# Performance work log

Measured on AMD Instinct MI355X. Metric: run time of the kernel, lower is better.

The kernel has to match this reference:

```python
import jax, jax.numpy as jnp
import numpy as np

N = 100000   # nodes
E = 1600000  # edges
D = 128      # d_model
H = 8        # heads
HD = D // H  # head dim
T = 8        # edge types


def setup_inputs() -> dict:
    key = jax.random.key(0)
    ks = jax.random.split(key, 16)
    s = 0.02
    inp = {
        "x": jax.random.normal(ks[0], (N, D), jnp.float32),
        "edge_index": jax.random.randint(ks[1], (2, E), 0, N, jnp.int32),
        "edge_type": jax.random.randint(ks[2], (E,), 0, T, jnp.int32),
        "Wq": jax.random.normal(ks[3], (D, D), jnp.float32) * s,
        "bq": jnp.zeros((D,), jnp.float32),
        "Wk": jax.random.normal(ks[4], (D, D), jnp.float32) * s,
        "bk": jnp.zeros((D,), jnp.float32),
        "Wv": jax.random.normal(ks[5], (D, D), jnp.float32) * s,
        "bv": jnp.zeros((D,), jnp.float32),
        "Wo": jax.random.normal(ks[6], (D, D), jnp.float32) * s,
        "bo": jnp.zeros((D,), jnp.float32),
        "edge_bias": jax.random.normal(ks[7], (T, H), jnp.float32) * s,
        "W1": jax.random.normal(ks[8], (D, D), jnp.float32) * s,
        "b1": jnp.zeros((D,), jnp.float32),
        "W2": jax.random.normal(ks[9], (D, D), jnp.float32) * s,
        "b2": jnp.zeros((D,), jnp.float32),
        "g1": jnp.ones((D,), jnp.float32),
        "be1": jnp.zeros((D,), jnp.float32),
        "g2": jnp.ones((D,), jnp.float32),
        "be2": jnp.zeros((D,), jnp.float32),
    }
    return inp


def _layernorm(x, g, b, eps=1e-5):
    m = jnp.mean(x, axis=-1, keepdims=True)
    v = jnp.mean((x - m) ** 2, axis=-1, keepdims=True)
    return (x - m) * jax.lax.rsqrt(v + eps) * g + b


def reference(x, edge_index, edge_type, Wq, bq, Wk, bk, Wv, bv, Wo, bo,
              edge_bias, W1, b1, W2, b2, g1, be1, g2, be2):
    n = x.shape[0]
    scale = HD ** -0.5
    Q = (x @ Wq + bq).reshape(n, H, HD)
    K = (x @ Wk + bk).reshape(n, H, HD)
    V = (x @ Wv + bv).reshape(n, H, HD)
    src, dst = edge_index[0], edge_index[1]
    # per-edge attention logits [E, H]
    attn = jnp.sum(Q[dst] * K[src], axis=-1) * scale + edge_bias[edge_type]
    # segment softmax grouped by destination node
    mx = jax.ops.segment_max(attn, dst, num_segments=n)  # [n, H]
    ex = jnp.exp(attn - mx[dst])
    sm = jax.ops.segment_sum(ex, dst, num_segments=n)
    a = ex / (sm[dst] + 1e-16)
    # weighted scatter-add of values
    out = jax.ops.segment_sum(a[..., None] * V[src], dst, num_segments=n)
    out = out.reshape(n, D) @ Wo + bo
    x = _layernorm(x + out, g1, be1)
    ffn = jax.nn.gelu(x @ W1 + b1, approximate=False) @ W2 + b2
    return _layernorm(x + ffn, g2, be2)
```

## Files before the change

### kernel.cpp

```cpp
#include <hip/hip_runtime.h>
#include <math.h>

#define D   128
#define NH  8
#define CAP 64
#define SCW 132

typedef __attribute__((ext_vector_type(8))) short  bfrag;
typedef __attribute__((ext_vector_type(4))) float  f32x4;
typedef __attribute__((ext_vector_type(8))) unsigned short u16x8;

__device__ __forceinline__ unsigned short f2bf(float f) {
  unsigned int u = __float_as_uint(f);
  unsigned int r = u + 0x7fffu + ((u >> 16) & 1u);
  return (unsigned short)(r >> 16);
}
__device__ __forceinline__ float bf2f(unsigned short b) {
  return __uint_as_float(((unsigned int)b) << 16);
}

__device__ __forceinline__ int swz(int r, int kb) {
  return r * 256 + (kb ^ ((r & 7) << 4));
}

__global__ void prew_kernel(const float* __restrict__ W0, const float* __restrict__ W1,
                            const float* __restrict__ W2, const float* __restrict__ W3,
                            const float* __restrict__ W4, const float* __restrict__ W5,
                            unsigned short* __restrict__ img)
{
  const float* Wm[6] = {W0, W1, W2, W3, W4, W5};
  const float* W = Wm[blockIdx.x];
  unsigned short* ih = img + (size_t)blockIdx.x * 32768;
  unsigned short* il = ih + 16384;
  for (int s = threadIdx.x; s < 16384; s += 256) {
    int j = s & 7, l = (s >> 3) & 63, kk = (s >> 9) & 3, cbg = s >> 11;
    int c = cbg * 16 + (l & 15);
    int k = kk * 32 + (l >> 4) * 8 + j;
    float v = W[k * D + c];
    unsigned short h = f2bf(v);
    ih[s] = h;
    il[s] = f2bf(v - bf2f(h));
  }
}

__device__ __forceinline__ void stage_x(const float* __restrict__ A, char* lds,
                                        int r0, int n, int t)
{
#pragma unroll
  for (int i = 0; i < 8; ++i) {
    int f = i * 256 + t;
    int r = f >> 5;
    int c = (f & 31) * 4;
    float4 v = make_float4(0.f, 0.f, 0.f, 0.f);
    int row = r0 + r;
    if (row < n) v = *(const float4*)&A[(size_t)row * D + c];
    unsigned short h0 = f2bf(v.x), h1 = f2bf(v.y), h2 = f2bf(v.z), h3 = f2bf(v.w);
    ushort4 hv; hv.x = h0; hv.y = h1; hv.z = h2; hv.w = h3;
    ushort4 lv;
    lv.x = f2bf(v.x - bf2f(h0)); lv.y = f2bf(v.y - bf2f(h1));
    lv.z = f2bf(v.z - bf2f(h2)); lv.w = f2bf(v.w - bf2f(h3));
    int o = swz(r, c * 2);
    *(ushort4*)(lds + o)         = hv;
    *(ushort4*)(lds + 16384 + o) = lv;
  }
}

__device__ __forceinline__ void gemm_tile(const unsigned short* __restrict__ imgh,
                                          const unsigned short* __restrict__ imgl,
                                          const char* lds, f32x4 (&acc)[4][2],
                                          int wave, int lane)
{
  bfrag bh[2][4], bl[2][4];
#pragma unroll
  for (int cb = 0; cb < 2; ++cb)
#pragma unroll
    for (int kk = 0; kk < 4; ++kk) {
      int f = ((wave * 2 + cb) * 4 + kk) * 64 + lane;
      bh[cb][kk] = *(const bfrag*)&imgh[f * 8];
      bl[cb][kk] = *(const bfrag*)&imgl[f * 8];
    }
#pragma unroll
  for (int rb = 0; rb < 4; ++rb)
#pragma unroll
    for (int kk = 0; kk < 4; ++kk) {
      int o = swz(rb * 16 + (lane & 15), kk * 64 + (lane >> 4) * 16);
      bfrag ah = *(const bfrag*)(lds + o);
      bfrag al = *(const bfrag*)(lds + 16384 + o);
#pragma unroll
      for (int cb = 0; cb < 2; ++cb) {
        acc[rb][cb] = __builtin_amdgcn_mfma_f32_16x16x32_bf16(ah, bh[cb][kk], acc[rb][cb], 0, 0, 0);
        acc[rb][cb] = __builtin_amdgcn_mfma_f32_16x16x32_bf16(al, bh[cb][kk], acc[rb][cb], 0, 0, 0);
        acc[rb][cb] = __builtin_amdgcn_mfma_f32_16x16x32_bf16(ah, bl[cb][kk], acc[rb][cb], 0, 0, 0);
      }
    }
}

__device__ __forceinline__ void zero_acc(f32x4 (&acc)[4][2]) {
#pragma unroll
  for (int rb = 0; rb < 4; ++rb)
#pragma unroll
    for (int cb = 0; cb < 2; ++cb) {
      f32x4 z = {0.f, 0.f, 0.f, 0.f};
      acc[rb][cb] = z;
    }
}

__device__ __forceinline__ void store_scF(const f32x4 (&acc)[4][2], float* scF,
                                          const float* __restrict__ bias,
                                          int wave, int lane)
{
  float b0 = bias[wave * 32 + (lane & 15)];
  float b1 = bias[wave * 32 + 16 + (lane & 15)];
#pragma unroll
  for (int rb = 0; rb < 4; ++rb)
#pragma unroll
    for (int cb = 0; cb < 2; ++cb) {
      float bb = cb ? b1 : b0;
      int col = wave * 32 + cb * 16 + (lane & 15);
#pragma unroll
      for (int r = 0; r < 4; ++r) {
        int row = rb * 16 + (lane >> 4) * 4 + r;
        scF[row * SCW + col] = acc[rb][cb][r] + bb;
      }
    }
}

__device__ __forceinline__ void write_bufA4(char* lds, int row, int tc,
                                            float v0, float v1, float v2, float v3)
{
  unsigned short h0 = f2bf(v0), h1 = f2bf(v1), h2 = f2bf(v2), h3 = f2bf(v3);
  ushort4 hv; hv.x = h0; hv.y = h1; hv.z = h2; hv.w = h3;
  ushort4 lv;
  lv.x = f2bf(v0 - bf2f(h0)); lv.y = f2bf(v1 - bf2f(h1));
  lv.z = f2bf(v2 - bf2f(h2)); lv.w = f2bf(v3 - bf2f(h3));
  int o = swz(row, tc * 8);
  *(ushort4*)(lds + o)         = hv;
  *(ushort4*)(lds + 16384 + o) = lv;
}

__global__ __launch_bounds__(256, 2) void qkv_kernel(
    const float* __restrict__ x, const unsigned short* __restrict__ img,
    const float* __restrict__ bq, const float* __restrict__ bk, const float* __restrict__ bv,
    unsigned short* __restrict__ Q, unsigned short* __restrict__ K,
    unsigned short* __restrict__ V, int n)
{
  __shared__ char lds[49152];
  const int t = threadIdx.x, wave = t >> 6, lane = t & 63;
  const int r0 = blockIdx.x * 64;
  stage_x(x, lds, r0, n, t);
  __syncthreads();

  const float* bs[3] = {bq, bk, bv};
  unsigned short* Os[3] = {Q, K, V};
  unsigned short* scH = (unsigned short*)(lds + 32768);

  for (int m = 0; m < 3; ++m) {
    f32x4 acc[4][2];
    zero_acc(acc);
    gemm_tile(img + (size_t)m * 32768, img + (size_t)m * 32768 + 16384, lds, acc, wave, lane);
    float b0 = bs[m][wave * 32 + (lane & 15)];
    float b1 = bs[m][wave * 32 + 16 + (lane & 15)];
    __syncthreads();
#pragma unroll
    for (int rb = 0; rb < 4; ++rb)
#pragma unroll
      for (int cb = 0; cb < 2; ++cb) {
        float bb = cb ? b1 : b0;
        int col = wave * 32 + cb * 16 + (lane & 15);
#pragma unroll
        for (int r = 0; r < 4; ++r) {
          int row = rb * 16 + (lane >> 4) * 4 + r;
          scH[row * D + col] = f2bf(acc[rb][cb][r] + bb);
        }
      }
    __syncthreads();
#pragma unroll
    for (int i = 0; i < 8; ++i) {
      int f = i * 256 + t;
      int row = f >> 5, c4 = (f & 31) * 4;
      if (r0 + row < n)
        *(ushort4*)&Os[m][(size_t)(r0 + row) * D + c4] = *(ushort4*)&scH[row * D + c4];
    }
  }
}

__global__ __launch_bounds__(256, 2) void ffn_kernel(
    const float* __restrict__ AO, const unsigned short* __restrict__ img,
    const float* __restrict__ x,
    const float* __restrict__ bo, const float* __restrict__ b1, const float* __restrict__ b2,
    const float* __restrict__ g1, const float* __restrict__ be1,
    const float* __restrict__ g2, const float* __restrict__ be2,
    float* __restrict__ out, int n)
{
  __shared__ char lds[32768 + 64 * SCW * 4];
  float* scF = (float*)(lds + 32768);
  const int t = threadIdx.x, wave = t >> 6, lane = t & 63;
  const int r0 = blockIdx.x * 64;
  const int tc = t & 31, tr = t >> 5;

  stage_x(AO, lds, r0, n, t);
  __syncthreads();

  f32x4 acc[4][2];

  zero_acc(acc);
  gemm_tile(img + 3 * 32768, img + 3 * 32768 + 16384, lds, acc, wave, lane);
  store_scF(acc, scF, bo, wave, lane);
  __syncthreads();

  float x1v[8][4];
  {
    float4 g4  = *(const float4*)&g1[tc * 4];
    float4 be4 = *(const float4*)&be1[tc * 4];
#pragma unroll
    for (int i = 0; i < 8; ++i) {
      int row = tr * 8 + i, grow = r0 + row;
      float4 y = *(float4*)&scF[row * SCW + tc * 4];
      float4 rv = make_float4(0.f, 0.f, 0.f, 0.f);
      if (grow < n) rv = *(const float4*)&x[(size_t)grow * D + tc * 4];
      float y0 = y.x + rv.x, y1 = y.y + rv.y, y2 = y.z + rv.z, y3 = y.w + rv.w;
      float sum = y0 + y1 + y2 + y3;
#pragma unroll
      for (int off = 16; off; off >>= 1) sum += __shfl_xor(sum, off);
      float mean = sum * (1.f / 128.f);
      float d0 = y0 - mean, d1 = y1 - mean, d2 = y2 - mean, d3 = y3 - mean;
      float sq = d0 * d0 + d1 * d1 + d2 * d2 + d3 * d3;
#pragma unroll
      for (int off = 16; off; off >>= 1) sq += __shfl_xor(sq, off);
      float inv = 1.0f / sqrtf(sq * (1.f / 128.f) + 1e-5f);
      float v0 = d0 * inv * g4.x + be4.x, v1 = d1 * inv * g4.y + be4.y;
      float v2 = d2 * inv * g4.z + be4.z, v3 = d3 * inv * g4.w + be4.w;
      x1v[i][0] = v0; x1v[i][1] = v1; x1v[i][2] = v2; x1v[i][3] = v3;
      write_bufA4(lds, row, tc, v0, v1, v2, v3);
    }
  }
  __syncthreads();

  zero_acc(acc);
  gemm_tile(img + 4 * 32768, img + 4 * 32768 + 16384, lds, acc, wave, lane);
  store_scF(acc, scF, b1, wave, lane);
  __syncthreads();
#pragma unroll
  for (int i = 0; i < 8; ++i) {
    int row = tr * 8 + i;
    float4 y = *(float4*)&scF[row * SCW + tc * 4];
    const float kc = 0.70710678118654752f;
    float v0 = 0.5f * y.x * (1.f + erff(y.x * kc));
    float v1 = 0.5f * y.y * (1.f + erff(y.y * kc));
    float v2 = 0.5f * y.z * (1.f + erff(y.z * kc));
    float v3 = 0.5f * y.w * (1.f + erff(y.w * kc));
    write_bufA4(lds, row, tc, v0, v1, v2, v3);
  }
  __syncthreads();

  zero_acc(acc);
  gemm_tile(img + 5 * 32768, img + 5 * 32768 + 16384, lds, acc, wave, lane);
  store_scF(acc, scF, b2, wave, lane);
  __syncthreads();
  {
    float4 g4  = *(const float4*)&g2[tc * 4];
    float4 be4 = *(const float4*)&be2[tc * 4];
#pragma unroll
    for (int i = 0; i < 8; ++i) {
      int row = tr * 8 + i, grow = r0 + row;
      float4 y = *(float4*)&scF[row * SCW + tc * 4];
      float y0 = y.x + x1v[i][0], y1 = y.y + x1v[i][1];
      float y2 = y.z + x1v[i][2], y3 = y.w + x1v[i][3];
      float sum = y0 + y1 + y2 + y3;
#pragma unroll
      for (int off = 16; off; off >>= 1) sum += __shfl_xor(sum, off);
      float mean = sum * (1.f / 128.f);
      float d0 = y0 - mean, d1 = y1 - mean, d2 = y2 - mean, d3 = y3 - mean;
      float sq = d0 * d0 + d1 * d1 + d2 * d2 + d3 * d3;
#pragma unroll
      for (int off = 16; off; off >>= 1) sq += __shfl_xor(sq, off);
      float inv = 1.0f / sqrtf(sq * (1.f / 128.f) + 1e-5f);
      if (grow < n) {
        float4 o;
        o.x = d0 * inv * g4.x + be4.x; o.y = d1 * inv * g4.y + be4.y;
        o.z = d2 * inv * g4.z + be4.z; o.w = d3 * inv * g4.w + be4.w;
        *(float4*)&out[(size_t)grow * D + tc * 4] = o;
      }
    }
  }
}

__global__ __launch_bounds__(256) void fill_kernel(
    const int* __restrict__ ei, const int* __restrict__ et,
    int* __restrict__ cnt, unsigned* __restrict__ bucket,
    int n, int e, int nper)
{
  const int xcd = blockIdx.x & 7;
  const int lo  = xcd * nper;
  const int nb  = gridDim.x >> 3;
  const int sl  = blockIdx.x >> 3;
  const int stride = nb * 256;
  for (int i = sl * 256 + threadIdx.x; i < e; i += stride) {
    int d = ei[e + i];
    if ((unsigned)(d - lo) < (unsigned)nper) {
      int s  = ei[i];
      int ty = et[i];
      int pos = atomicAdd(&cnt[d], 1);
      if (pos < CAP) bucket[(size_t)d * CAP + pos] = (unsigned)s | ((unsigned)ty << 24);
    }
  }
}

__global__ __launch_bounds__(256) void attn_kernel(
    const unsigned short* __restrict__ Q, const unsigned short* __restrict__ K,
    const unsigned short* __restrict__ V, const float* __restrict__ ebias,
    const int* __restrict__ cnt, const unsigned* __restrict__ bucket,
    float* __restrict__ out, int n)
{
  __shared__ float eb_s[64];
  if (threadIdx.x < 64) eb_s[threadIdx.x] = ebias[threadIdx.x];
  __syncthreads();

  const int wave = threadIdx.x >> 6, lane = threadIdx.x & 63;
  const int node = blockIdx.x * 4 + wave;
  if (node >= n) return;

  const int g  = lane >> 4;
  const int l  = lane & 15;
  const int d0 = l * 8;
  const int h  = l >> 1;

  int deg = cnt[node];
  if (deg > CAP) deg = CAP;

  unsigned packed = 0u;
  if (lane < deg) packed = bucket[(size_t)node * CAP + lane];

  u16x8 qv = *(const u16x8*)&Q[(size_t)node * D + d0];
  float q[8];
#pragma unroll
  for (int i = 0; i < 8; ++i) q[i] = bf2f(qv[i]) * 0.25f;

  float s = 0.f, a[8];
#pragma unroll
  for (int i = 0; i < 8; ++i) a[i] = 0.f;

  for (int j = 0; j < deg; j += 4) {
    int slot = j + g;
    unsigned cur = __shfl(packed, slot < 63 ? slot : 63);
    int src = (int)(cur & 0xFFFFFFu);
    int ty  = (int)(cur >> 24);
    u16x8 kv = *(const u16x8*)&K[(size_t)src * D + d0];
    u16x8 vv = *(const u16x8*)&V[(size_t)src * D + d0];
    float dot = 0.f;
#pragma unroll
    for (int i = 0; i < 8; ++i) dot += q[i] * bf2f(kv[i]);
    dot += __shfl_xor(dot, 1);
    float logit = dot + eb_s[ty * NH + h];
    float p = (slot < deg) ? __expf(logit) : 0.f;
    s += p;
#pragma unroll
    for (int i = 0; i < 8; ++i) a[i] += p * bf2f(vv[i]);
  }
  s += __shfl_xor(s, 16); s += __shfl_xor(s, 32);
#pragma unroll
  for (int i = 0; i < 8; ++i) { a[i] += __shfl_xor(a[i], 16); a[i] += __shfl_xor(a[i], 32); }

  if (g == 0) {
    float inv = 1.f / (s + 1e-16f);
    float4 o0 = make_float4(a[0] * inv, a[1] * inv, a[2] * inv, a[3] * inv);
    float4 o1 = make_float4(a[4] * inv, a[5] * inv, a[6] * inv, a[7] * inv);
    *(float4*)&out[(size_t)node * D + d0]     = o0;
    *(float4*)&out[(size_t)node * D + d0 + 4] = o1;
  }
}

extern "C" void kernel_launch(void* const* d_in, const int* in_sizes, int n_in,
                              void* d_out, int out_size, void* d_ws, size_t ws_size,
                              hipStream_t stream)
{
  const float* x   = (const float*)d_in[0];
  const int*   ei  = (const int*)  d_in[1];
  const int*   et  = (const int*)  d_in[2];
  const float* Wq  = (const float*)d_in[3];
  const float* bq  = (const float*)d_in[4];
  const float* Wk  = (const float*)d_in[5];
  const float* bk  = (const float*)d_in[6];
  const float* Wv  = (const float*)d_in[7];
  const float* bv  = (const float*)d_in[8];
  const float* Wo  = (const float*)d_in[9];
  const float* bo  = (const float*)d_in[10];
  const float* eb  = (const float*)d_in[11];
  const float* W1  = (const float*)d_in[12];
  const float* b1  = (const float*)d_in[13];
  const float* W2  = (const float*)d_in[14];
  const float* b2  = (const float*)d_in[15];
  const float* g1  = (const float*)d_in[16];
  const float* be1 = (const float*)d_in[17];
  const float* g2  = (const float*)d_in[18];
  const float* be2 = (const float*)d_in[19];

  const int n = in_sizes[0] / D;
  const int e = in_sizes[2];
  const size_t nd = (size_t)n * D;

  unsigned short* Qb = (unsigned short*)d_ws;
  unsigned short* Kb = Qb + nd;
  unsigned short* Vb = Kb + nd;
  float*    AO     = (float*)(Vb + nd);
  unsigned* bucket = (unsigned*)(AO + nd);
  int*      cnt    = (int*)(bucket + (size_t)n * CAP);
  unsigned short* img = (unsigned short*)(cnt + n);

  hipMemsetAsync(cnt, 0, (size_t)n * sizeof(int), stream);

  const int gb = (n + 63) / 64;
  const int nper = (n + 7) / 8;
  prew_kernel<<<6, 256, 0, stream>>>(Wq, Wk, Wv, Wo, W1, W2, img);
  fill_kernel<<<2048, 256, 0, stream>>>(ei, et, cnt, bucket, n, e, nper);
  qkv_kernel<<<gb, 256, 0, stream>>>(x, img, bq, bk, bv, Qb, Kb, Vb, n);
  attn_kernel<<<(n + 3) / 4, 256, 0, stream>>>(Qb, Kb, Vb, eb, cnt, bucket, AO, n);
  ffn_kernel<<<gb, 256, 0, stream>>>(AO, img, x, bo, b1, b2, g1, be1, g2, be2,
                                     (float*)d_out, n);
}
```

Before: 488.8 us.

## Store K in FP8 and merge edge bucketing into the QKV kernel launch

K is now written as FP8 (e4m3 via the cvt_pk_fp8 builtin) instead of bf16, which halves the bytes gathered per edge for the key in the attention kernel. The attention kernel unpacks the FP8 values with cvt_pk_f32_fp8. The edge-bucketing fill work moves into extra blocks of the QKV GEMM launch so the two run concurrently, and the separate launch goes away. FP8 keys lose precision in the attention logits, which may push the error past tolerance, and the fill blocks' loop stride is hardcoded to 65536 assuming 2048 blocks.

```diff
diff --git a/kernel.cpp b/kernel.cpp
--- a/kernel.cpp
+++ b/kernel.cpp
@@ -8,6 +8,7 @@
 
 typedef __attribute__((ext_vector_type(8))) short  bfrag;
 typedef __attribute__((ext_vector_type(4))) float  f32x4;
+typedef __attribute__((ext_vector_type(2))) float  f32x2;
 typedef __attribute__((ext_vector_type(8))) unsigned short u16x8;
 
 __device__ __forceinline__ unsigned short f2bf(float f) {
@@ -138,21 +139,40 @@
   *(ushort4*)(lds + 16384 + o) = lv;
 }
 
-__global__ __launch_bounds__(256, 2) void qkv_kernel(
+__global__ __launch_bounds__(256, 2) void qkvf_kernel(
     const float* __restrict__ x, const unsigned short* __restrict__ img,
     const float* __restrict__ bq, const float* __restrict__ bk, const float* __restrict__ bv,
-    unsigned short* __restrict__ Q, unsigned short* __restrict__ K,
-    unsigned short* __restrict__ V, int n)
+    unsigned short* __restrict__ Q, unsigned char* __restrict__ K8,
+    unsigned short* __restrict__ V, int n, int gb,
+    const int* __restrict__ ei, const int* __restrict__ et,
+    int* __restrict__ cnt, unsigned* __restrict__ bucket, int e, int nper)
 {
   __shared__ char lds[49152];
-  const int t = threadIdx.x, wave = t >> 6, lane = t & 63;
+  const int t = threadIdx.x;
+
+  if ((int)blockIdx.x >= gb) {
+    const int bid = blockIdx.x - gb;
+    const int xcd = bid & 7;
+    const int lo  = xcd * nper;
+    const int sl  = bid >> 3;
+    for (int i = sl * 256 + t; i < e; i += 65536) {
+      int d = ei[e + i];
+      if ((unsigned)(d - lo) < (unsigned)nper) {
+        int s  = ei[i];
+        int ty = et[i];
+        int pos = atomicAdd(&cnt[d], 1);
+        if (pos < CAP) bucket[(size_t)d * CAP + pos] = (unsigned)s | ((unsigned)ty << 24);
+      }
+    }
+    return;
+  }
+
+  const int wave = t >> 6, lane = t & 63;
   const int r0 = blockIdx.x * 64;
   stage_x(x, lds, r0, n, t);
   __syncthreads();
 
   const float* bs[3] = {bq, bk, bv};
-  unsigned short* Os[3] = {Q, K, V};
-  unsigned short* scH = (unsigned short*)(lds + 32768);
 
   for (int m = 0; m < 3; ++m) {
     f32x4 acc[4][2];
@@ -161,25 +181,53 @@
     float b0 = bs[m][wave * 32 + (lane & 15)];
     float b1 = bs[m][wave * 32 + 16 + (lane & 15)];
     __syncthreads();
-#pragma unroll
-    for (int rb = 0; rb < 4; ++rb)
-#pragma unroll
-      for (int cb = 0; cb < 2; ++cb) {
-        float bb = cb ? b1 : b0;
-        int col = wave * 32 + cb * 16 + (lane & 15);
-#pragma unroll
-        for (int r = 0; r < 4; ++r) {
-          int row = rb * 16 + (lane >> 4) * 4 + r;
-          scH[row * D + col] = f2bf(acc[rb][cb][r] + bb);
+    if (m == 1) {
+      unsigned char* scB = (unsigned char*)(lds + 32768);
+#pragma unroll
+      for (int rb = 0; rb < 4; ++rb)
+#pragma unroll
+        for (int cb = 0; cb < 2; ++cb) {
+          float bb = cb ? b1 : b0;
+          int col = wave * 32 + cb * 16 + (lane & 15);
+#pragma unroll
+          for (int r = 0; r < 4; ++r) {
+            int row = rb * 16 + (lane >> 4) * 4 + r;
+            float v = acc[rb][cb][r] + bb;
+            unsigned p = (unsigned)__builtin_amdgcn_cvt_pk_fp8_f32(v, v, 0, false);
+            scB[row * 128 + col] = (unsigned char)(p & 0xFF);
+          }
         }
-      }
-    __syncthreads();
-#pragma unroll
-    for (int i = 0; i < 8; ++i) {
-      int f = i * 256 + t;
-      int row = f >> 5, c4 = (f & 31) * 4;
-      if (r0 + row < n)
-        *(ushort4*)&Os[m][(size_t)(r0 + row) * D + c4] = *(ushort4*)&scH[row * D + c4];
+      __syncthreads();
+#pragma unroll
+      for (int i = 0; i < 8; ++i) {
+        int idx = i * 256 + t;
+        int row = idx >> 5, c4 = (idx & 31) * 4;
+        if (r0 + row < n)
+          *(unsigned*)&K8[(size_t)(r0 + row) * 128 + c4] = *(unsigned*)&scB[row * 128 + c4];
+      }
+    } else {
+      unsigned short* scH = (unsigned short*)(lds + 32768);
+      unsigned short* O = (m == 0) ? Q : V;
+#pragma unroll
+      for (int rb = 0; rb < 4; ++rb)
+#pragma unroll
+        for (int cb = 0; cb < 2; ++cb) {
+          float bb = cb ? b1 : b0;
+          int col = wave * 32 + cb * 16 + (lane & 15);
+#pragma unroll
+          for (int r = 0; r < 4; ++r) {
+            int row = rb * 16 + (lane >> 4) * 4 + r;
+            scH[row * D + col] = f2bf(acc[rb][cb][r] + bb);
+          }
+        }
+      __syncthreads();
+#pragma unroll
+      for (int i = 0; i < 8; ++i) {
+        int f = i * 256 + t;
+        int row = f >> 5, c4 = (f & 31) * 4;
+        if (r0 + row < n)
+          *(ushort4*)&O[(size_t)(r0 + row) * D + c4] = *(ushort4*)&scH[row * D + c4];
+      }
     }
   }
 }
@@ -285,29 +333,8 @@
   }
 }
 
-__global__ __launch_bounds__(256) void fill_kernel(
-    const int* __restrict__ ei, const int* __restrict__ et,
-    int* __restrict__ cnt, unsigned* __restrict__ bucket,
-    int n, int e, int nper)
-{
-  const int xcd = blockIdx.x & 7;
-  const int lo  = xcd * nper;
-  const int nb  = gridDim.x >> 3;
-  const int sl  = blockIdx.x >> 3;
-  const int stride = nb * 256;
-  for (int i = sl * 256 + threadIdx.x; i < e; i += stride) {
-    int d = ei[e + i];
-    if ((unsigned)(d - lo) < (unsigned)nper) {
-      int s  = ei[i];
-      int ty = et[i];
-      int pos = atomicAdd(&cnt[d], 1);
-      if (pos < CAP) bucket[(size_t)d * CAP + pos] = (unsigned)s | ((unsigned)ty << 24);
-    }
-  }
-}
-
 __global__ __launch_bounds__(256) void attn_kernel(
-    const unsigned short* __restrict__ Q, const unsigned short* __restrict__ K,
+    const unsigned short* __restrict__ Q, const unsigned char* __restrict__ K8,
     const unsigned short* __restrict__ V, const float* __restrict__ ebias,
     const int* __restrict__ cnt, const unsigned* __restrict__ bucket,
     float* __restrict__ out, int n)
@@ -345,11 +372,14 @@
     unsigned cur = __shfl(packed, slot < 63 ? slot : 63);
     int src = (int)(cur & 0xFFFFFFu);
     int ty  = (int)(cur >> 24);
-    u16x8 kv = *(const u16x8*)&K[(size_t)src * D + d0];
+    uint2 kw = *(const uint2*)&K8[(size_t)src * 128 + d0];
     u16x8 vv = *(const u16x8*)&V[(size_t)src * D + d0];
-    float dot = 0.f;
-#pragma unroll
-    for (int i = 0; i < 8; ++i) dot += q[i] * bf2f(kv[i]);
+    f32x2 k01 = __builtin_amdgcn_cvt_pk_f32_fp8((int)kw.x, false);
+    f32x2 k23 = __builtin_amdgcn_cvt_pk_f32_fp8((int)kw.x, true);
+    f32x2 k45 = __builtin_amdgcn_cvt_pk_f32_fp8((int)kw.y, false);
+    f32x2 k67 = __builtin_amdgcn_cvt_pk_f32_fp8((int)kw.y, true);
+    float dot = q[0] * k01[0] + q[1] * k01[1] + q[2] * k23[0] + q[3] * k23[1]
+              + q[4] * k45[0] + q[5] * k45[1] + q[6] * k67[0] + q[7] * k67[1];
     dot += __shfl_xor(dot, 1);
     float logit = dot + eb_s[ty * NH + h];
     float p = (slot < deg) ? __expf(logit) : 0.f;
@@ -400,9 +430,9 @@
   const size_t nd = (size_t)n * D;
 
   unsigned short* Qb = (unsigned short*)d_ws;
-  unsigned short* Kb = Qb + nd;
-  unsigned short* Vb = Kb + nd;
-  float*    AO     = (float*)(Vb + nd);
+  unsigned short* Vb = Qb + nd;
+  unsigned char*  K8 = (unsigned char*)(Vb + nd);
+  float*    AO     = (float*)(K8 + nd);
   unsigned* bucket = (unsigned*)(AO + nd);
   int*      cnt    = (int*)(bucket + (size_t)n * CAP);
   unsigned short* img = (unsigned short*)(cnt + n);
@@ -412,9 +442,9 @@
   const int gb = (n + 63) / 64;
   const int nper = (n + 7) / 8;
   prew_kernel<<<6, 256, 0, stream>>>(Wq, Wk, Wv, Wo, W1, W2, img);
-  fill_kernel<<<2048, 256, 0, stream>>>(ei, et, cnt, bucket, n, e, nper);
-  qkv_kernel<<<gb, 256, 0, stream>>>(x, img, bq, bk, bv, Qb, Kb, Vb, n);
-  attn_kernel<<<(n + 3) / 4, 256, 0, stream>>>(Qb, Kb, Vb, eb, cnt, bucket, AO, n);
+  qkvf_kernel<<<gb + 2048, 256, 0, stream>>>(x, img, bq, bk, bv, Qb, K8, Vb, n, gb,
+                                             ei, et, cnt, bucket, e, nper);
+  attn_kernel<<<(n + 3) / 4, 256, 0, stream>>>(Qb, K8, Vb, eb, cnt, bucket, AO, n);
   ffn_kernel<<<gb, 256, 0, stream>>>(AO, img, x, bo, b1, b2, g1, be1, g2, be2,
                                      (float*)d_out, n);
 }
```

Result: slower. 546.1 us (+11.7%).
